# Kernel optimization log

Measured on AMD Instinct MI355X. Metric: run time of the kernel, lower is better.

Reference implementation:

```python
import jax, jax.numpy as jnp
import numpy as np

D_IN, D, SEQ, B = 512, 1024, 2048, 8
EPS = 1e-5


def positional_encoding(seq_len, d):
    pos = np.arange(seq_len)[:, None].astype(np.float32)
    i = np.arange(d)[None, :].astype(np.float32)
    angle_rads = pos / (10000.0 ** (2.0 * np.floor(i / 2.0) / np.float32(d)))
    angle_rads[:, 0::2] = np.sin(angle_rads[:, 0::2])
    angle_rads[:, 1::2] = np.cos(angle_rads[:, 1::2])
    return jnp.asarray(angle_rads[None, ...], dtype=jnp.float32)  # [1, s, d]


def setup_inputs() -> dict:
    key = jax.random.key(0)
    ks = jax.random.split(key, 10)
    def lin(k, fan_in, shape):
        bound = 1.0 / np.sqrt(fan_in)
        return jax.random.uniform(k, shape, jnp.float32, -bound, bound)
    return {
        "inputs": jax.random.normal(ks[0], (B, SEQ, D_IN), jnp.float32),
        "embed_w": lin(ks[1], D_IN, (D, D_IN)),
        "embed_b": lin(ks[2], D_IN, (D,)),
        "wq_w": lin(ks[3], D, (D, D)), "wq_b": lin(ks[3], D, (D,)),
        "wk_w": lin(ks[4], D, (D, D)), "wk_b": lin(ks[4], D, (D,)),
        "wv_w": lin(ks[5], D, (D, D)), "wv_b": lin(ks[5], D, (D,)),
        "ln_g": jnp.ones((D,), jnp.float32),
        "ln_b": jnp.zeros((D,), jnp.float32),
        "soft_key_w": lin(ks[6], D, (D, D)),
        "soft_query": jax.random.normal(ks[7], (D,), jnp.float32),
        "pos_enc": positional_encoding(SEQ, D),
    }


def reference(inputs, embed_w, embed_b, wq_w, wq_b, wk_w, wk_b, wv_w, wv_b,
              ln_g, ln_b, soft_key_w, soft_query, pos_enc):
    x = jnp.einsum('bsi,oi->bso', inputs, embed_w) + embed_b  # embed
    x = x + pos_enc  # broadcast positional encoding over batch
    Q = jnp.einsum('bsd,od->bso', x, wq_w) + wq_b
    K = jnp.einsum('bsd,od->bso', x, wk_w) + wk_b
    V = jnp.einsum('bsd,od->bso', x, wv_w) + wv_b
    score = jnp.einsum('bso,bio->bsi', Q, K) / jnp.sqrt(jnp.float32(D))
    score = jax.nn.softmax(score, axis=2)
    Z = jnp.einsum('bsi,bio->bso', score, V)
    h = x + Z
    mu = jnp.mean(h, axis=-1, keepdims=True)
    var = jnp.mean(jnp.square(h - mu), axis=-1, keepdims=True)
    H = (h - mu) * jax.lax.rsqrt(var + EPS) * ln_g + ln_b
    soft_key = jnp.tanh(jnp.einsum('bsd,od->bso', H, soft_key_w))
    soft_score = jax.nn.softmax(jnp.einsum('bso,o->bs', soft_key, soft_query), axis=1)
    return jnp.einsum('bs,bso->bo', soft_score, H)
```

## Files before the change

### kernel.cpp

```cpp
#include <hip/hip_runtime.h>
#include <hip/hip_bf16.h>
#include <math.h>

typedef __bf16 bf16_t;
typedef bf16_t bf16x8 __attribute__((ext_vector_type(8)));
typedef bf16_t bf16x4 __attribute__((ext_vector_type(4)));
typedef float  f32x4  __attribute__((ext_vector_type(4)));

#define D_IN   512
#define DMODEL 1024
#define SEQ    2048
#define BATCH  8
#define NTOK   (BATCH*SEQ)

typedef __attribute__((address_space(1))) unsigned int gu32;
typedef __attribute__((address_space(3))) unsigned int lu32;

__device__ __forceinline__ void async16(const void* g, void* l) {
    __builtin_amdgcn_global_load_lds((gu32*)g, (lu32*)l, 16, 0, 0);
}

template<int EPI>
__global__ __launch_bounds__(256)
void gemm_bt(const bf16_t* __restrict__ Ab, const bf16_t* __restrict__ Bb,
             bf16_t* __restrict__ Cb, int K, int ldc, int gx, int gy,
             long batchA, long batchB, long batchC,
             const float* __restrict__ bias, const float* __restrict__ aux_f,
             const bf16_t* __restrict__ resid, float* __restrict__ logits,
             const float* __restrict__ bias3)
{
    __shared__ __align__(16) bf16_t smem[32768];

    const int tid  = threadIdx.x;
    const int lane = tid & 63;
    const int wave = tid >> 6;

    const int flat = blockIdx.x;
    const int nb   = gridDim.x;
    const int vid  = (flat & 7) * (nb >> 3) + (flat >> 3);
    const int pb   = gx * gy;
    const int z    = vid / pb;
    const int w    = vid - z * pb;
    const int sy   = w / (gx * 4);
    const int r    = w - sy * (gx * 4);
    const int sx   = r >> 4;
    const int inner= r & 15;
    const int mtile = (sy * 4 + (inner & 3)) * 128;
    const int ntile = (sx * 4 + (inner >> 2)) * 128;

    const bf16_t* A  = Ab + (long)z * batchA;
    const bf16_t* Bp = Bb + (long)z * batchB;

    f32x4 acc[4][4];
    #pragma unroll
    for (int i = 0; i < 4; ++i)
        #pragma unroll
        for (int j = 0; j < 4; ++j)
            acc[i][j] = (f32x4)(0.f);

    const int lr  = lane & 15;
    const int lr7 = lr & 7;
    const int lq  = lane >> 4;

    const int wrow = (wave >> 1) * 64;
    const int wcol = (wave & 1) * 64;

    const int srow8 = lane >> 3;
    const int sk    = ((lane & 7) ^ srow8) * 8;

    {
        bf16_t* Ad = smem;
        bf16_t* Bd = smem + 8192;
        #pragma unroll
        for (int j = 0; j < 4; ++j) {
            const int g   = (wave << 2) + j;
            const int row = (g << 3) + srow8;
            async16(A  + (long)(mtile + row) * K + sk, &Ad[g << 9]);
            async16(Bp + (long)(ntile + row) * K + sk, &Bd[g << 9]);
        }
    }

    int cur = 0;
    for (int k0 = 0; k0 < K; k0 += 64) {
        __syncthreads();
        if (k0 + 64 < K) {
            bf16_t* Ad = smem + ((cur ^ 1) << 14);
            bf16_t* Bd = Ad + 8192;
            const int kn = k0 + 64;
            #pragma unroll
            for (int j = 0; j < 4; ++j) {
                const int g   = (wave << 2) + j;
                const int row = (g << 3) + srow8;
                async16(A  + (long)(mtile + row) * K + (kn + sk), &Ad[g << 9]);
                async16(Bp + (long)(ntile + row) * K + (kn + sk), &Bd[g << 9]);
            }
        }
        const bf16_t* Ar = smem + (cur << 14);
        const bf16_t* Br = Ar + 8192;
        #pragma unroll
        for (int s = 0; s < 2; ++s) {
            const int po = ((lq + (s << 2)) ^ lr7) << 3;
            bf16x8 af[4], bf[4];
            #pragma unroll
            for (int t = 0; t < 4; ++t)
                af[t] = *(const bf16x8*)&Ar[(wrow + t*16 + lr)*64 + po];
            #pragma unroll
            for (int t = 0; t < 4; ++t)
                bf[t] = *(const bf16x8*)&Br[(wcol + t*16 + lr)*64 + po];
            #pragma unroll
            for (int tr = 0; tr < 4; ++tr)
                #pragma unroll
                for (int tc = 0; tc < 4; ++tc)
                    acc[tr][tc] = __builtin_amdgcn_mfma_f32_16x16x32_bf16(
                                      af[tr], bf[tc], acc[tr][tc], 0, 0, 0);
        }
        cur ^= 1;
    }

    if constexpr (EPI == 5) {
        const int mbase = mtile + wrow + lq*4;
        #pragma unroll
        for (int tr = 0; tr < 4; ++tr) {
            #pragma unroll
            for (int reg = 0; reg < 4; ++reg) {
                const int m = mbase + tr*16 + reg;
                float rs = 0.f;
                #pragma unroll
                for (int tc = 0; tc < 4; ++tc) {
                    const int n = ntile + wcol + tc*16 + lr;
                    rs += tanhf(acc[tr][tc][reg]) * aux_f[n];
                }
                rs += __shfl_xor(rs, 1);
                rs += __shfl_xor(rs, 2);
                rs += __shfl_xor(rs, 4);
                rs += __shfl_xor(rs, 8);
                if (lr == 0) atomicAdd(&logits[m], rs);
            }
        }
        return;
    }

    __syncthreads();

    if constexpr (EPI == 4) {
        float* fsm = (float*)smem;
        #pragma unroll
        for (int tr = 0; tr < 4; ++tr) {
            #pragma unroll
            for (int reg = 0; reg < 4; ++reg) {
                const int rl = wrow + tr*16 + lq*4 + reg;
                #pragma unroll
                for (int tc = 0; tc < 4; ++tc) {
                    const int cl = wcol + tc*16 + lr;
                    fsm[rl*128 + ((((cl >> 2) ^ (rl & 31)) << 2) | (cl & 3))] = acc[tr][tc][reg];
                }
            }
        }
        __syncthreads();
        bf16_t* C = Cb + (long)z * batchC;
        const int chunk = tid & 15;
        const int grp   = tid >> 4;
        #pragma unroll
        for (int rep = 0; rep < 8; ++rep) {
            const int R  = grp + rep*16;
            const int c0 = chunk*8;
            const int p0 = (((c0 >> 2)       ^ (R & 31)) << 2);
            const int p1 = ((((c0 + 4) >> 2) ^ (R & 31)) << 2);
            const f32x4 f0 = *(const f32x4*)&fsm[R*128 + p0];
            const f32x4 f1 = *(const f32x4*)&fsm[R*128 + p1];
            const long off = (long)(mtile + R)*ldc + ntile + c0;
            const bf16x8 r8 = *(const bf16x8*)&resid[(long)z*batchC + off];
            bf16x8 val;
            #pragma unroll
            for (int i = 0; i < 4; ++i) {
                val[i]     = (bf16_t)(f0[i] + (float)r8[i]);
                val[i + 4] = (bf16_t)(f1[i] + (float)r8[i + 4]);
            }
            *(bf16x8*)&C[off] = val;
        }
        return;
    }

    const int seg = (EPI == 6) ? (ntile >> 10) : 0;
    const float* bp = bias;
    if constexpr (EPI == 6) bp = (seg == 0) ? bias : (seg == 1) ? aux_f : bias3;

    #pragma unroll
    for (int tr = 0; tr < 4; ++tr) {
        #pragma unroll
        for (int reg = 0; reg < 4; ++reg) {
            const int rl = wrow + tr*16 + lq*4 + reg;
            #pragma unroll
            for (int tc = 0; tc < 4; ++tc) {
                const int cl = wcol + tc*16 + lr;
                float v = acc[tr][tc][reg];
                if constexpr (EPI == 0)
                    v += bias[ntile + cl] + aux_f[((mtile + rl) & (SEQ-1))*DMODEL + ntile + cl];
                if constexpr (EPI == 3) v *= 0.03125f;
                if constexpr (EPI == 6) v += bp[(ntile + cl) & 1023];
                smem[rl*128 + ((((cl >> 3) ^ (rl & 7)) << 3) | (cl & 7))] = (bf16_t)v;
            }
        }
    }
    __syncthreads();

    if constexpr (EPI == 6) {
        if (seg == 2) {
            bf16_t* VTb = Cb + 33554432;
            const int col  = tid & 127;
            const int half = tid >> 7;
            const int b    = mtile >> 11, s0 = mtile & (SEQ-1);
            const long nbase = (long)b*DMODEL + (ntile & 1023) + col;
            #pragma unroll
            for (int rep = 0; rep < 8; ++rep) {
                const int R0 = half*64 + rep*8;
                bf16x8 o;
                #pragma unroll
                for (int i = 0; i < 8; ++i) {
                    const int rl = R0 + i;
                    o[i] = smem[rl*128 + ((((col >> 3) ^ (rl & 7)) << 3) | (col & 7))];
                }
                *(bf16x8*)&VTb[nbase*SEQ + s0 + R0] = o;
            }
            return;
        }
        const int chunk = tid & 15;
        const int grp   = tid >> 4;
        const long base = (long)seg * 16777216 + (ntile & 1023) + chunk*8;
        #pragma unroll
        for (int rep = 0; rep < 8; ++rep) {
            const int R = grp + rep*16;
            const int phys = chunk ^ (R & 7);
            bf16x8 val = *(const bf16x8*)&smem[R*128 + phys*8];
            *(bf16x8*)&Cb[base + (long)(mtile + R)*1024] = val;
        }
        return;
    }

    bf16_t* C = Cb + (long)z * batchC;
    const int chunk = tid & 15;
    const int grp   = tid >> 4;
    #pragma unroll
    for (int rep = 0; rep < 8; ++rep) {
        const int R = grp + rep*16;
        const int phys = chunk ^ (R & 7);
        bf16x8 val = *(const bf16x8*)&smem[R*128 + phys*8];
        const long off = (long)(mtile + R)*ldc + ntile + chunk*8;
        *(bf16x8*)&C[off] = val;
    }
}

__global__ __launch_bounds__(256) void cast_all(
        const float* __restrict__ inp, const float* __restrict__ emw,
        const float* __restrict__ wqw, const float* __restrict__ wkw,
        const float* __restrict__ wvw, const float* __restrict__ skw,
        bf16_t* __restrict__ in_b, bf16_t* __restrict__ we_b,
        bf16_t* __restrict__ wq_b, bf16_t* __restrict__ wk_b,
        bf16_t* __restrict__ wv_b, bf16_t* __restrict__ sk_b,
        float* __restrict__ logits) {
    const int i = blockIdx.x*256 + threadIdx.x;
    const float* s; bf16_t* d; int j;
    if      (i < 2097152) { s = inp; d = in_b; j = i; }
    else if (i < 2228224) { s = emw; d = we_b; j = i - 2097152; }
    else if (i < 2490368) { s = wqw; d = wq_b; j = i - 2228224; }
    else if (i < 2752512) { s = wkw; d = wk_b; j = i - 2490368; }
    else if (i < 3014656) { s = wvw; d = wv_b; j = i - 2752512; }
    else if (i < 3276800) { s = skw; d = sk_b; j = i - 3014656; }
    else {
        if (i < 3280896) ((f32x4*)logits)[i - 3276800] = (f32x4)(0.f);
        return;
    }
    const float4 f = ((const float4*)s)[j];
    bf16x4 o;
    o[0] = (bf16_t)f.x; o[1] = (bf16_t)f.y; o[2] = (bf16_t)f.z; o[3] = (bf16_t)f.w;
    ((bf16x4*)d)[j] = o;
}

__global__ __launch_bounds__(256) void softmax_rows_bf16(bf16_t* __restrict__ P) {
    bf16_t* row = P + (long)blockIdx.x * SEQ;
    const int t = threadIdx.x, lane = t & 63, wave = t >> 6;
    __shared__ float sm[8];
    const bf16x8 hv = *(const bf16x8*)&row[t*8];
    float v[8]; float mx = -3.0e38f;
    #pragma unroll
    for (int j = 0; j < 8; ++j) { v[j] = (float)hv[j]; mx = fmaxf(mx, v[j]); }
    #pragma unroll
    for (int o = 32; o; o >>= 1) mx = fmaxf(mx, __shfl_xor(mx, o));
    if (lane == 0) sm[wave] = mx;
    __syncthreads();
    mx = fmaxf(fmaxf(sm[0], sm[1]), fmaxf(sm[2], sm[3]));
    float s = 0.f;
    #pragma unroll
    for (int j = 0; j < 8; ++j) { v[j] = __expf(v[j] - mx); s += v[j]; }
    #pragma unroll
    for (int o = 32; o; o >>= 1) s += __shfl_xor(s, o);
    if (lane == 0) sm[4 + wave] = s;
    __syncthreads();
    s = (sm[4] + sm[5]) + (sm[6] + sm[7]);
    const float inv = 1.f / s;
    bf16x8 o8;
    #pragma unroll
    for (int j = 0; j < 8; ++j) o8[j] = (bf16_t)(v[j] * inv);
    *(bf16x8*)&row[t*8] = o8;
}

__global__ __launch_bounds__(256) void layernorm_k(const bf16_t* __restrict__ h, bf16_t* __restrict__ H,
                                                   const float* __restrict__ gam, const float* __restrict__ bet) {
    const long row = blockIdx.x;
    const bf16_t* hr = h + row*DMODEL;
    bf16_t* Hr = H + row*DMODEL;
    const int t = threadIdx.x, lane = t & 63, wave = t >> 6;
    __shared__ float sm[8];
    const bf16x4 hv = *(const bf16x4*)&hr[t*4];
    float v[4]; float s = 0.f, q = 0.f;
    #pragma unroll
    for (int j = 0; j < 4; ++j) { v[j] = (float)hv[j]; s += v[j]; q += v[j]*v[j]; }
    #pragma unroll
    for (int o = 32; o; o >>= 1) { s += __shfl_xor(s, o); q += __shfl_xor(q, o); }
    if (lane == 0) { sm[wave] = s; sm[4 + wave] = q; }
    __syncthreads();
    s = (sm[0] + sm[1]) + (sm[2] + sm[3]);
    q = (sm[4] + sm[5]) + (sm[6] + sm[7]);
    const float mu  = s * (1.f/DMODEL);
    const float var = q * (1.f/DMODEL) - mu*mu;
    const float r   = rsqrtf(var + 1e-5f);
    const float4 g4 = ((const float4*)gam)[t];
    const float4 b4 = ((const float4*)bet)[t];
    bf16x4 o4;
    o4[0] = (bf16_t)((v[0] - mu)*r*g4.x + b4.x);
    o4[1] = (bf16_t)((v[1] - mu)*r*g4.y + b4.y);
    o4[2] = (bf16_t)((v[2] - mu)*r*g4.z + b4.z);
    o4[3] = (bf16_t)((v[3] - mu)*r*g4.w + b4.w);
    *(bf16x4*)&Hr[t*4] = o4;
}

__global__ __launch_bounds__(256) void pool_partial(const float* __restrict__ logits,
                                                    const bf16_t* __restrict__ H,
                                                    float* __restrict__ part) {
    const int b = blockIdx.y;
    const int c = blockIdx.x;
    const int t = threadIdx.x, lane = t & 63, wave = t >> 6;
    __shared__ float sm[8];
    __shared__ float wsm[32];
    const float* lb = logits + b*SEQ;
    const float4 a4 = ((const float4*)lb)[t];
    const float4 c4 = ((const float4*)lb)[t + 256];
    float v[8] = {a4.x, a4.y, a4.z, a4.w, c4.x, c4.y, c4.z, c4.w};
    float mx = -3.0e38f;
    #pragma unroll
    for (int j = 0; j < 8; ++j) mx = fmaxf(mx, v[j]);
    #pragma unroll
    for (int o = 32; o; o >>= 1) mx = fmaxf(mx, __shfl_xor(mx, o));
    if (lane == 0) sm[wave] = mx;
    __syncthreads();
    mx = fmaxf(fmaxf(sm[0], sm[1]), fmaxf(sm[2], sm[3]));
    float s = 0.f;
    #pragma unroll
    for (int j = 0; j < 8; ++j) s += __expf(v[j] - mx);
    #pragma unroll
    for (int o = 32; o; o >>= 1) s += __shfl_xor(s, o);
    if (lane == 0) sm[4 + wave] = s;
    __syncthreads();
    s = (sm[4] + sm[5]) + (sm[6] + sm[7]);
    const float inv = 1.f / s;
    if (t < 32) wsm[t] = __expf(lb[c*32 + t] - mx) * inv;
    __syncthreads();

    const bf16_t* Hb = H + ((long)b*SEQ + (long)c*32)*DMODEL;
    f32x4 acc = (f32x4)(0.f);
    #pragma unroll 4
    for (int i = 0; i < 32; ++i) {
        const float wi = wsm[i];
        const bf16x4 hv = *(const bf16x4*)&Hb[(long)i*DMODEL + t*4];
        acc[0] += wi * (float)hv[0];
        acc[1] += wi * (float)hv[1];
        acc[2] += wi * (float)hv[2];
        acc[3] += wi * (float)hv[3];
    }
    *(f32x4*)&part[((long)b*64 + c)*DMODEL + t*4] = acc;
}

__global__ __launch_bounds__(256) void pool_reduce(const float* __restrict__ part,
                                                   float* __restrict__ out) {
    const int i = blockIdx.x*256 + threadIdx.x;
    const int b = i >> 10, o = i & 1023;
    const float* p = part + (long)b*64*DMODEL + o;
    float s = 0.f;
    #pragma unroll
    for (int c = 0; c < 64; ++c) s += p[c*DMODEL];
    out[i] = s;
}

extern "C" void kernel_launch(void* const* d_in, const int* in_sizes, int n_in,
                              void* d_out, int out_size, void* d_ws, size_t ws_size,
                              hipStream_t stream) {
    (void)in_sizes; (void)n_in; (void)out_size; (void)ws_size;
    const float* inp = (const float*)d_in[0];
    const float* emw = (const float*)d_in[1];
    const float* emb = (const float*)d_in[2];
    const float* wqw = (const float*)d_in[3];
    const float* wqb = (const float*)d_in[4];
    const float* wkw = (const float*)d_in[5];
    const float* wkb = (const float*)d_in[6];
    const float* wvw = (const float*)d_in[7];
    const float* wvb = (const float*)d_in[8];
    const float* lng = (const float*)d_in[9];
    const float* lnb = (const float*)d_in[10];
    const float* skw = (const float*)d_in[11];
    const float* sq  = (const float*)d_in[12];
    const float* pos = (const float*)d_in[13];
    float* out = (float*)d_out;

    char* ws = (char*)d_ws;
    bf16_t* in_b   = (bf16_t*)(ws + 0);
    bf16_t* we_b   = (bf16_t*)(ws + 16777216);
    bf16_t* wq_b   = (bf16_t*)(ws + 17825792);
    bf16_t* wk_b   = (bf16_t*)(ws + 19922944);
    bf16_t* wv_b   = (bf16_t*)(ws + 22020096);
    bf16_t* sk_b   = (bf16_t*)(ws + 24117248);
    float*  logits = (float*)(ws + 26214400);
    bf16_t* xb     = (bf16_t*)(ws + 26345472);
    bf16_t* Qb     = (bf16_t*)(ws + 59899904);
    bf16_t* Kb     = (bf16_t*)(ws + 93454336);
    bf16_t* VT     = (bf16_t*)(ws + 127008768);
    bf16_t* Hb     = (bf16_t*)(ws + 160563200);
    bf16_t* Pb     = (bf16_t*)(ws + 194117632);
    float*  part   = (float*)(ws + 0);

    cast_all<<<12816, 256, 0, stream>>>(inp, emw, wqw, wkw, wvw, skw,
                                        in_b, we_b, wq_b, wk_b, wv_b, sk_b, logits);

    gemm_bt<0><<<1024, 256, 0, stream>>>(in_b, we_b, xb, D_IN, DMODEL, 8, 128,
        0, 0, 0, emb, pos, nullptr, nullptr, nullptr);
    gemm_bt<6><<<3072, 256, 0, stream>>>(xb, wq_b, Qb, DMODEL, DMODEL, 24, 128,
        0, 0, 0, wqb, wkb, nullptr, nullptr, wvb);
    gemm_bt<3><<<2048, 256, 0, stream>>>(Qb, Kb, Pb, DMODEL, SEQ, 16, 16,
        (long)SEQ*DMODEL, (long)SEQ*DMODEL, (long)SEQ*SEQ, nullptr, nullptr, nullptr, nullptr, nullptr);
    softmax_rows_bf16<<<NTOK, 256, 0, stream>>>(Pb);
    gemm_bt<4><<<1024, 256, 0, stream>>>(Pb, VT, Qb, SEQ, DMODEL, 8, 16,
        (long)SEQ*SEQ, (long)DMODEL*SEQ, (long)SEQ*DMODEL, nullptr, nullptr, xb, nullptr, nullptr);
    layernorm_k<<<NTOK, 256, 0, stream>>>(Qb, Hb, lng, lnb);
    gemm_bt<5><<<1024, 256, 0, stream>>>(Hb, sk_b, nullptr, DMODEL, 0, 8, 128,
        0, 0, 0, nullptr, sq, nullptr, logits, nullptr);
    pool_partial<<<dim3(64, BATCH), 256, 0, stream>>>(logits, Hb, part);
    pool_reduce<<<32, 256, 0, stream>>>(part, out);
}
```

Baseline: 518.9 us.

## Fuse softmax into score GEMM epilogue with deferred row normalization

Drops the separate row-softmax kernel. The QK^T GEMM epilogue now writes exp(score) directly and builds per-row sums with atomics, and the PV GEMM epilogue divides by the row sum before adding the residual. This saves one full read and write pass over the large bf16 score matrix and one kernel launch. The cost is that max subtraction is skipped, so exp can overflow for large scores, and the atomic row-sum accumulation adds contention and makes the result order-dependent.

```diff
diff --git a/kernel.cpp b/kernel.cpp
--- a/kernel.cpp
+++ b/kernel.cpp
@@ -158,6 +158,7 @@
         }
         __syncthreads();
         bf16_t* C = Cb + (long)z * batchC;
+        const float* rsum = bias + (long)z * SEQ;
         const int chunk = tid & 15;
         const int grp   = tid >> 4;
         #pragma unroll
@@ -168,13 +169,14 @@
             const int p1 = ((((c0 + 4) >> 2) ^ (R & 31)) << 2);
             const f32x4 f0 = *(const f32x4*)&fsm[R*128 + p0];
             const f32x4 f1 = *(const f32x4*)&fsm[R*128 + p1];
+            const float inv = 1.f / rsum[mtile + R];
             const long off = (long)(mtile + R)*ldc + ntile + c0;
             const bf16x8 r8 = *(const bf16x8*)&resid[(long)z*batchC + off];
             bf16x8 val;
             #pragma unroll
             for (int i = 0; i < 4; ++i) {
-                val[i]     = (bf16_t)(f0[i] + (float)r8[i]);
-                val[i + 4] = (bf16_t)(f1[i] + (float)r8[i + 4]);
+                val[i]     = (bf16_t)(f0[i]*inv + (float)r8[i]);
+                val[i + 4] = (bf16_t)(f1[i]*inv + (float)r8[i + 4]);
             }
             *(bf16x8*)&C[off] = val;
         }
@@ -196,13 +198,37 @@
                 float v = acc[tr][tc][reg];
                 if constexpr (EPI == 0)
                     v += bias[ntile + cl] + aux_f[((mtile + rl) & (SEQ-1))*DMODEL + ntile + cl];
-                if constexpr (EPI == 3) v *= 0.03125f;
+                if constexpr (EPI == 3) v = __expf(v * 0.03125f);
                 if constexpr (EPI == 6) v += bp[(ntile + cl) & 1023];
                 smem[rl*128 + ((((cl >> 3) ^ (rl & 7)) << 3) | (cl & 7))] = (bf16_t)v;
             }
         }
     }
     __syncthreads();
+
+    if constexpr (EPI == 3) {
+        bf16_t* C = Cb + (long)z * batchC;
+        float* rsum = logits + (long)z * SEQ;
+        const int chunk = tid & 15;
+        const int grp   = tid >> 4;
+        #pragma unroll
+        for (int rep = 0; rep < 8; ++rep) {
+            const int R = grp + rep*16;
+            const int phys = chunk ^ (R & 7);
+            bf16x8 val = *(const bf16x8*)&smem[R*128 + phys*8];
+            const long off = (long)(mtile + R)*ldc + ntile + chunk*8;
+            *(bf16x8*)&C[off] = val;
+            float ps = 0.f;
+            #pragma unroll
+            for (int i = 0; i < 8; ++i) ps += (float)val[i];
+            ps += __shfl_xor(ps, 1);
+            ps += __shfl_xor(ps, 2);
+            ps += __shfl_xor(ps, 4);
+            ps += __shfl_xor(ps, 8);
+            if (chunk == 0) atomicAdd(&rsum[mtile + R], ps);
+        }
+        return;
+    }
 
     if constexpr (EPI == 6) {
         if (seg == 2) {
@@ -257,7 +283,7 @@
         bf16_t* __restrict__ in_b, bf16_t* __restrict__ we_b,
         bf16_t* __restrict__ wq_b, bf16_t* __restrict__ wk_b,
         bf16_t* __restrict__ wv_b, bf16_t* __restrict__ sk_b,
-        float* __restrict__ logits) {
+        float* __restrict__ logits, float* __restrict__ rowsum) {
     const int i = blockIdx.x*256 + threadIdx.x;
     const float* s; bf16_t* d; int j;
     if      (i < 2097152) { s = inp; d = in_b; j = i; }
@@ -266,42 +292,12 @@
     else if (i < 2752512) { s = wkw; d = wk_b; j = i - 2490368; }
     else if (i < 3014656) { s = wvw; d = wv_b; j = i - 2752512; }
     else if (i < 3276800) { s = skw; d = sk_b; j = i - 3014656; }
-    else {
-        if (i < 3280896) ((f32x4*)logits)[i - 3276800] = (f32x4)(0.f);
-        return;
-    }
+    else if (i < 3280896) { ((f32x4*)logits)[i - 3276800] = (f32x4)(0.f); return; }
+    else                  { ((f32x4*)rowsum)[i - 3280896] = (f32x4)(0.f); return; }
     const float4 f = ((const float4*)s)[j];
     bf16x4 o;
     o[0] = (bf16_t)f.x; o[1] = (bf16_t)f.y; o[2] = (bf16_t)f.z; o[3] = (bf16_t)f.w;
     ((bf16x4*)d)[j] = o;
-}
-
-__global__ __launch_bounds__(256) void softmax_rows_bf16(bf16_t* __restrict__ P) {
-    bf16_t* row = P + (long)blockIdx.x * SEQ;
-    const int t = threadIdx.x, lane = t & 63, wave = t >> 6;
-    __shared__ float sm[8];
-    const bf16x8 hv = *(const bf16x8*)&row[t*8];
-    float v[8]; float mx = -3.0e38f;
-    #pragma unroll
-    for (int j = 0; j < 8; ++j) { v[j] = (float)hv[j]; mx = fmaxf(mx, v[j]); }
-    #pragma unroll
-    for (int o = 32; o; o >>= 1) mx = fmaxf(mx, __shfl_xor(mx, o));
-    if (lane == 0) sm[wave] = mx;
-    __syncthreads();
-    mx = fmaxf(fmaxf(sm[0], sm[1]), fmaxf(sm[2], sm[3]));
-    float s = 0.f;
-    #pragma unroll
-    for (int j = 0; j < 8; ++j) { v[j] = __expf(v[j] - mx); s += v[j]; }
-    #pragma unroll
-    for (int o = 32; o; o >>= 1) s += __shfl_xor(s, o);
-    if (lane == 0) sm[4 + wave] = s;
-    __syncthreads();
-    s = (sm[4] + sm[5]) + (sm[6] + sm[7]);
-    const float inv = 1.f / s;
-    bf16x8 o8;
-    #pragma unroll
-    for (int j = 0; j < 8; ++j) o8[j] = (bf16_t)(v[j] * inv);
-    *(bf16x8*)&row[t*8] = o8;
 }
 
 __global__ __launch_bounds__(256) void layernorm_k(const bf16_t* __restrict__ h, bf16_t* __restrict__ H,
@@ -419,6 +415,7 @@
     bf16_t* wv_b   = (bf16_t*)(ws + 22020096);
     bf16_t* sk_b   = (bf16_t*)(ws + 24117248);
     float*  logits = (float*)(ws + 26214400);
+    float*  rowsum = (float*)(ws + 26279936);
     bf16_t* xb     = (bf16_t*)(ws + 26345472);
     bf16_t* Qb     = (bf16_t*)(ws + 59899904);
     bf16_t* Kb     = (bf16_t*)(ws + 93454336);
@@ -427,18 +424,18 @@
     bf16_t* Pb     = (bf16_t*)(ws + 194117632);
     float*  part   = (float*)(ws + 0);
 
-    cast_all<<<12816, 256, 0, stream>>>(inp, emw, wqw, wkw, wvw, skw,
-                                        in_b, we_b, wq_b, wk_b, wv_b, sk_b, logits);
+    cast_all<<<12832, 256, 0, stream>>>(inp, emw, wqw, wkw, wvw, skw,
+                                        in_b, we_b, wq_b, wk_b, wv_b, sk_b,
+                                        logits, rowsum);
 
     gemm_bt<0><<<1024, 256, 0, stream>>>(in_b, we_b, xb, D_IN, DMODEL, 8, 128,
         0, 0, 0, emb, pos, nullptr, nullptr, nullptr);
     gemm_bt<6><<<3072, 256, 0, stream>>>(xb, wq_b, Qb, DMODEL, DMODEL, 24, 128,
         0, 0, 0, wqb, wkb, nullptr, nullptr, wvb);
     gemm_bt<3><<<2048, 256, 0, stream>>>(Qb, Kb, Pb, DMODEL, SEQ, 16, 16,
-        (long)SEQ*DMODEL, (long)SEQ*DMODEL, (long)SEQ*SEQ, nullptr, nullptr, nullptr, nullptr, nullptr);
-    softmax_rows_bf16<<<NTOK, 256, 0, stream>>>(Pb);
+        (long)SEQ*DMODEL, (long)SEQ*DMODEL, (long)SEQ*SEQ, nullptr, nullptr, nullptr, rowsum, nullptr);
     gemm_bt<4><<<1024, 256, 0, stream>>>(Pb, VT, Qb, SEQ, DMODEL, 8, 16,
-        (long)SEQ*SEQ, (long)DMODEL*SEQ, (long)SEQ*DMODEL, nullptr, nullptr, xb, nullptr, nullptr);
+        (long)SEQ*SEQ, (long)DMODEL*SEQ, (long)SEQ*DMODEL, rowsum, nullptr, xb, nullptr, nullptr);
     layernorm_k<<<NTOK, 256, 0, stream>>>(Qb, Hb, lng, lnb);
     gemm_bt<5><<<1024, 256, 0, stream>>>(Hb, sk_b, nullptr, DMODEL, 0, 8, 128,
         0, 0, 0, nullptr, sq, nullptr, logits, nullptr);
```

After: 515.9 us. No clear change (-0.6%).
